# Optimization experiments

Measured on AMD Instinct MI355X. Metric: run time of the kernel, lower is better.

## Reference

```python
import jax, jax.numpy as jnp
import numpy as np

B, NQ, NKV = 16, 4096, 77
QUERY_DIM, CONTEXT_DIM = 320, 768
HEADS, DIM_HEAD = 8, 64
INNER = HEADS * DIM_HEAD
SCALE = DIM_HEAD ** (-0.5)
MAX_NEG = -jnp.finfo(jnp.float32).max / 2


def setup_inputs() -> dict:
    key = jax.random.key(0)
    ks = jax.random.split(key, 8)
    x = jax.random.normal(ks[0], (B, NQ, QUERY_DIM), dtype=jnp.float32)
    context = jax.random.normal(ks[1], (B, NKV, CONTEXT_DIM), dtype=jnp.float32)
    mask = jax.random.randint(ks[2], (B, 1, 1, NKV), 0, 2).astype(bool)
    s = 0.02
    Wq = jax.random.normal(ks[3], (QUERY_DIM, INNER), dtype=jnp.float32) * s
    Wk = jax.random.normal(ks[4], (CONTEXT_DIM, INNER), dtype=jnp.float32) * s
    Wv = jax.random.normal(ks[5], (CONTEXT_DIM, INNER), dtype=jnp.float32) * s
    Wo = jax.random.normal(ks[6], (INNER, QUERY_DIM), dtype=jnp.float32) * s
    bo = jnp.zeros((QUERY_DIM,), dtype=jnp.float32)
    return {"x": x, "context": context, "mask": mask,
            "Wq": Wq, "Wk": Wk, "Wv": Wv, "Wo": Wo, "bo": bo}


def reference(x, context, mask, Wq, Wk, Wv, Wo, bo):
    # projections (bias-free Linears)
    q = (x @ Wq).reshape(B, NQ, HEADS, DIM_HEAD)        # b q h d
    k = (context @ Wk).reshape(B, NKV, HEADS, DIM_HEAD)  # b k h d
    v = (context @ Wv).reshape(B, NKV, HEADS, DIM_HEAD)  # b k h d
    # additive mask bias: 0 where mask, -finfo.max/2 where ~mask (matches masked_fill_)
    bias = jnp.where(mask, jnp.float32(0), MAX_NEG)      # broadcast to b h q k
    sim = jnp.einsum('bqhd,bkhd->bhqk', q, k) * SCALE + bias
    attn = jax.nn.softmax(sim, axis=-1)
    out = jnp.einsum('bhqk,bkhd->bqhd', attn, v).reshape(B, NQ, INNER)
    return out @ Wo + bo  # dropout p=0 -> identity
```

## Files before the change

### kernel.cpp

```cpp
#include <hip/hip_runtime.h>

typedef unsigned short ushort_t;
typedef __attribute__((ext_vector_type(8))) short bf16x8;
typedef __attribute__((ext_vector_type(4))) float f32x4;

#define B_SZ   16
#define NQ     4096
#define NKV    77
#define QDIM   320
#define CDIM   768
#define HEADS  8
#define DHEAD  64
#define INNER  512
#define M_ROWS (B_SZ * NQ)
#define VT_STR 104

__device__ __forceinline__ ushort_t f2bf(float f) {
  unsigned u = __builtin_bit_cast(unsigned, f);
  u = (u + 0x7fffu + ((u >> 16) & 1u)) >> 16;
  return (ushort_t)u;
}

__device__ __forceinline__ void async16(const ushort_t* g, ushort_t* l) {
  __builtin_amdgcn_global_load_lds(
      (const __attribute__((address_space(1))) unsigned int*)g,
      (__attribute__((address_space(3))) unsigned int*)l,
      16, 0, 0);
}

__global__ void mask_bias_kernel(const unsigned char* __restrict__ mraw,
                                 float* __restrict__ biasT) {
  __shared__ int s_u8, s_w4;
  if (threadIdx.x == 0) { s_u8 = 0; s_w4 = 0; }
  __syncthreads();
  const int nbytes = B_SZ * NKV;
  for (int i = threadIdx.x; i < nbytes; i += blockDim.x) {
    unsigned char v = mraw[i];
    if (v && (i & 3)) atomicOr(&s_u8, 1);
    if (v && ((i & 7) == 4)) atomicOr(&s_w4, 1);
  }
  __syncthreads();
  int mode = s_u8 ? 0 : (s_w4 ? 1 : 2);
  for (int i = threadIdx.x; i < B_SZ * 80; i += blockDim.x) {
    int b = i / 80, kv = i - b * 80;
    float bias = -2e30f;
    if (kv < NKV) {
      int idx = b * NKV + kv;
      long long m;
      if (mode == 0)      m = (long long)mraw[idx];
      else if (mode == 1) m = (long long)((const int*)mraw)[idx];
      else                m = ((const long long*)mraw)[idx];
      bias = m ? 0.0f : -1e30f;
    }
    biasT[i] = bias;
  }
}

__global__ void cast_f32_bf16(const float* __restrict__ in,
                              ushort_t* __restrict__ out, int n4) {
  int i = blockIdx.x * blockDim.x + threadIdx.x;
  int stride = gridDim.x * blockDim.x;
  const float4* in4 = (const float4*)in;
  ushort4* out4 = (ushort4*)out;
  for (; i < n4; i += stride) {
    float4 v = in4[i];
    ushort4 o;
    o.x = f2bf(v.x); o.y = f2bf(v.y); o.z = f2bf(v.z); o.w = f2bf(v.w);
    out4[i] = o;
  }
}

__global__ void tcast_f32_bf16(const float* __restrict__ in,
                               ushort_t* __restrict__ out,
                               int K, int N, int Npad, float scale) {
  int i = blockIdx.x * blockDim.x + threadIdx.x;
  int stride = gridDim.x * blockDim.x;
  int total = Npad * K;
  for (; i < total; i += stride) {
    int n = i / K, k = i - n * K;
    out[i] = (n < N) ? f2bf(in[(size_t)k * N + n] * scale) : (ushort_t)0;
  }
}

__global__ void vtrans_kernel(const ushort_t* __restrict__ kvb,
                              ushort_t* __restrict__ vt) {
  const int h = blockIdx.y, b = blockIdx.z;
  const int wid = threadIdx.x >> 6, lane = threadIdx.x & 63;
  const int d = blockIdx.x * 4 + wid;
  ushort_t* dst = vt + (size_t)(b * HEADS + h) * (64 * VT_STR) + d * VT_STR;
  for (int kv = lane; kv < VT_STR; kv += 64)
    dst[kv] = (kv < NKV)
        ? kvb[(size_t)(b * NKV + kv) * 1024 + 512 + h * 64 + d]
        : (ushort_t)0;
}

__global__ __launch_bounds__(256) void gemm_bf16(
    const ushort_t* __restrict__ A, const ushort_t* __restrict__ Bt,
    ushort_t* __restrict__ Cb,
    int K, int Astride, int Bstride, int Cstride) {
  __shared__ ushort_t As[128 * 64];
  __shared__ ushort_t Bs[128 * 64];
  const int tid = threadIdx.x;
  const int wid = tid >> 6, lane = tid & 63;
  const int wr = wid >> 1, wc = wid & 1;
  const int tileM = blockIdx.x * 128, tileN = blockIdx.y * 128;

  f32x4 acc[4][4];
#pragma unroll
  for (int m = 0; m < 4; ++m)
#pragma unroll
    for (int n = 0; n < 4; ++n) acc[m][n] = (f32x4){0.f, 0.f, 0.f, 0.f};

  const int srow = lane >> 3;
  const int scol = (lane & 7) * 8;

  for (int kt = 0; kt < K; kt += 64) {
    __syncthreads();
#pragma unroll
    for (int j = 0; j < 4; ++j) {
      int s = wid * 4 + j;
      const ushort_t* ga = A + (size_t)(tileM + s * 8 + srow) * Astride + kt + scol;
      const ushort_t* gb = Bt + (size_t)(tileN + s * 8 + srow) * Bstride + kt + scol;
      async16(ga, As + s * 512);
      async16(gb, Bs + s * 512);
    }
    __syncthreads();
#pragma unroll
    for (int kc = 0; kc < 2; ++kc) {
      bf16x8 af[4], bfr[4];
#pragma unroll
      for (int m = 0; m < 4; ++m)
        af[m] = *(const bf16x8*)&As[(wr * 64 + m * 16 + (lane & 15)) * 64 + kc * 32 + (lane >> 4) * 8];
#pragma unroll
      for (int n = 0; n < 4; ++n)
        bfr[n] = *(const bf16x8*)&Bs[(wc * 64 + n * 16 + (lane & 15)) * 64 + kc * 32 + (lane >> 4) * 8];
#pragma unroll
      for (int m = 0; m < 4; ++m)
#pragma unroll
        for (int n = 0; n < 4; ++n)
          acc[m][n] = __builtin_amdgcn_mfma_f32_16x16x32_bf16(af[m], bfr[n], acc[m][n], 0, 0, 0);
    }
  }

  const int r0 = tileM + wr * 64;
  const int c0 = tileN + wc * 64;
  const int rl2 = (lane >> 4) * 4;
  const int cl = lane & 15;
#pragma unroll
  for (int m = 0; m < 4; ++m)
#pragma unroll
    for (int n = 0; n < 4; ++n) {
      int col = c0 + n * 16 + cl;
#pragma unroll
      for (int r = 0; r < 4; ++r)
        Cb[(size_t)(r0 + m * 16 + rl2 + r) * Cstride + col] = f2bf(acc[m][n][r]);
    }
}

__global__ __launch_bounds__(512, 2) void gemm_qproj(
    const float* __restrict__ x, const ushort_t* __restrict__ Wt,
    ushort_t* __restrict__ qb) {
  __shared__ ushort_t As[2][128 * 32];
  __shared__ ushort_t Bs[2][512 * 32];
  const int tid = threadIdx.x;
  const int wid = tid >> 6, lane = tid & 63;
  const int wr = wid & 1, wc = wid >> 1;
  const int rl = lane & 15, kh = (lane >> 4) * 8;
  const int tileM = blockIdx.x * 128;

  f32x4 acc[4][8];
#pragma unroll
  for (int m = 0; m < 4; ++m)
#pragma unroll
    for (int n = 0; n < 8; ++n) acc[m][n] = (f32x4){0.f, 0.f, 0.f, 0.f};

  const int arow = tid >> 3;
  const int ac4 = tid & 7;
  const float4* x4 = (const float4*)x;
  float4 pa0, pa1;

#define QP_ISSUE_A(KT)                                                        \
  {                                                                           \
    size_t base = (size_t)(tileM + arow) * 80 + ((KT) >> 2) + ac4;            \
    pa0 = x4[base];                                                           \
    pa1 = x4[base + (size_t)64 * 80];                                         \
  }
#define QP_WRITE_A(BUF)                                                       \
  {                                                                           \
    ushort4 u0, u1;                                                           \
    u0.x = f2bf(pa0.x); u0.y = f2bf(pa0.y); u0.z = f2bf(pa0.z); u0.w = f2bf(pa0.w); \
    u1.x = f2bf(pa1.x); u1.y = f2bf(pa1.y); u1.z = f2bf(pa1.z); u1.w = f2bf(pa1.w); \
    *(ushort4*)&As[BUF][arow * 32 + ac4 * 4] = u0;                            \
    *(ushort4*)&As[BUF][(arow + 64) * 32 + ac4 * 4] = u1;                     \
  }
#define QP_STAGE_B(BUF, KT)                                                   \
  _Pragma("unroll")                                                           \
  for (int i = 0; i < 4; ++i) {                                               \
    int chunk = tid + i * 512;                                                \
    int n = chunk >> 2, c8 = chunk & 3;                                       \
    async16(Wt + (size_t)n * QDIM + (KT) + c8 * 8, &Bs[BUF][chunk * 8]);      \
  }

  QP_ISSUE_A(0)
  QP_WRITE_A(0)
  QP_STAGE_B(0, 0)
  __syncthreads();

  for (int s = 0; s < 10; ++s) {
    const int cur = s & 1;
    if (s < 9) {
      QP_ISSUE_A((s + 1) * 32)
      QP_STAGE_B(cur ^ 1, (s + 1) * 32)
    }
    bf16x8 af[4], bfr[8];
#pragma unroll
    for (int m = 0; m < 4; ++m)
      af[m] = *(const bf16x8*)&As[cur][(wr * 64 + m * 16 + rl) * 32 + kh];
#pragma unroll
    for (int n = 0; n < 8; ++n)
      bfr[n] = *(const bf16x8*)&Bs[cur][(wc * 128 + n * 16 + rl) * 32 + kh];
#pragma unroll
    for (int m = 0; m < 4; ++m)
#pragma unroll
      for (int n = 0; n < 8; ++n)
        acc[m][n] = __builtin_amdgcn_mfma_f32_16x16x32_bf16(af[m], bfr[n], acc[m][n], 0, 0, 0);
    if (s < 9) QP_WRITE_A(cur ^ 1)
    __syncthreads();
  }

  const int r0 = tileM + wr * 64;
  const int c0 = wc * 128;
  const int rl2 = (lane >> 4) * 4, cl = lane & 15;
#pragma unroll
  for (int m = 0; m < 4; ++m)
#pragma unroll
    for (int n = 0; n < 8; ++n)
#pragma unroll
      for (int r = 0; r < 4; ++r)
        qb[(size_t)(r0 + m * 16 + rl2 + r) * INNER + c0 + n * 16 + cl] = f2bf(acc[m][n][r]);
}

__global__ __launch_bounds__(512, 2) void gemm_oproj(
    const ushort_t* __restrict__ A, const ushort_t* __restrict__ Wt,
    const float* __restrict__ bo, float* __restrict__ out) {
  __shared__ ushort_t As[2][128 * 64];
  __shared__ ushort_t Bs[2][384 * 64];
  const int tid = threadIdx.x;
  const int wid = tid >> 6, lane = tid & 63;
  const int wr = wid & 1, wc = wid >> 1;
  const int rl = lane & 15, kh = (lane >> 4) * 8;
  const int tileM = blockIdx.x * 128;

  f32x4 acc[4][6];
#pragma unroll
  for (int m = 0; m < 4; ++m)
#pragma unroll
    for (int n = 0; n < 6; ++n) acc[m][n] = (f32x4){0.f, 0.f, 0.f, 0.f};

#define OP_STAGE(BUF, KT)                                                     \
  _Pragma("unroll")                                                           \
  for (int i = 0; i < 2; ++i) {                                               \
    int chunk = tid + i * 512;                                                \
    int row = chunk >> 3, c8 = chunk & 7;                                     \
    async16(A + (size_t)(tileM + row) * INNER + (KT) + c8 * 8,                \
            &As[BUF][chunk * 8]);                                             \
  }                                                                           \
  _Pragma("unroll")                                                           \
  for (int i = 0; i < 6; ++i) {                                               \
    int chunk = tid + i * 512;                                                \
    int n = chunk >> 3, c8 = chunk & 7;                                       \
    async16(Wt + (size_t)n * INNER + (KT) + c8 * 8, &Bs[BUF][chunk * 8]);     \
  }

  OP_STAGE(0, 0)
  __syncthreads();

  for (int s = 0; s < 8; ++s) {
    const int cur = s & 1;
    if (s < 7) { OP_STAGE(cur ^ 1, (s + 1) * 64) }
#pragma unroll
    for (int kc = 0; kc < 2; ++kc) {
      bf16x8 af[4], bfr[6];
#pragma unroll
      for (int m = 0; m < 4; ++m)
        af[m] = *(const bf16x8*)&As[cur][(wr * 64 + m * 16 + rl) * 64 + kc * 32 + kh];
#pragma unroll
      for (int n = 0; n < 6; ++n)
        bfr[n] = *(const bf16x8*)&Bs[cur][(wc * 96 + n * 16 + rl) * 64 + kc * 32 + kh];
#pragma unroll
      for (int m = 0; m < 4; ++m)
#pragma unroll
        for (int n = 0; n < 6; ++n)
          acc[m][n] = __builtin_amdgcn_mfma_f32_16x16x32_bf16(af[m], bfr[n], acc[m][n], 0, 0, 0);
    }
    __syncthreads();
  }

  const int r0 = tileM + wr * 64;
  const int c0 = wc * 96;
  const int rl2 = (lane >> 4) * 4, cl = lane & 15;
#pragma unroll
  for (int n = 0; n < 6; ++n) {
    int col = c0 + n * 16 + cl;
    if (col < QDIM) {
      float bv = bo[col];
#pragma unroll
      for (int m = 0; m < 4; ++m)
#pragma unroll
        for (int r = 0; r < 4; ++r)
          out[(size_t)(r0 + m * 16 + rl2 + r) * QDIM + col] = acc[m][n][r] + bv;
    }
  }
}

__global__ __launch_bounds__(256) void attn_kernel(
    const ushort_t* __restrict__ qb, const ushort_t* __restrict__ kvb,
    const ushort_t* __restrict__ vt, const float* __restrict__ biasT,
    ushort_t* __restrict__ ab) {
  __shared__ ushort_t Vt[64 * VT_STR];
  __shared__ ushort_t P[4 * 16 * VT_STR];
  const int qt = blockIdx.x, h = blockIdx.y, b = blockIdx.z;
  const int tid = threadIdx.x, wid = tid >> 6, lane = tid & 63;
  const int rl = lane & 15;
  const int kh = (lane >> 4) * 8;

  const ushort_t* vtg = vt + (size_t)(b * HEADS + h) * (64 * VT_STR);
  for (int i = tid; i < 832; i += 256) async16(vtg + i * 8, Vt + i * 8);
  for (int i = tid; i < 832; i += 256)
    *(bf16x8*)&P[i * 8] = (bf16x8){0, 0, 0, 0, 0, 0, 0, 0};

  bf16x8 kf[5][2];
  float bias_v[5];
#pragma unroll
  for (int nt = 0; nt < 5; ++nt) {
    int kv = nt * 16 + rl;
    bias_v[nt] = biasT[b * 80 + kv];
    kf[nt][0] = (bf16x8){0, 0, 0, 0, 0, 0, 0, 0};
    kf[nt][1] = (bf16x8){0, 0, 0, 0, 0, 0, 0, 0};
    if (kv < NKV) {
      const ushort_t* kp = &kvb[(size_t)(b * NKV + kv) * 1024 + h * 64 + kh];
      kf[nt][0] = *(const bf16x8*)kp;
      kf[nt][1] = *(const bf16x8*)(kp + 32);
    }
  }
  __syncthreads();

  const int qbase = b * NQ + qt * 256;
  const int pbase = wid * (16 * VT_STR);
#pragma unroll 1
  for (int chunk = 0; chunk < 4; ++chunk) {
    if (chunk) __syncthreads();
    const int row0 = chunk * 64 + wid * 16;

    const ushort_t* qp = &qb[(size_t)(qbase + row0 + rl) * INNER + h * 64 + kh];
    bf16x8 qf0 = *(const bf16x8*)qp;
    bf16x8 qf1 = *(const bf16x8*)(qp + 32);

    f32x4 s[5];
#pragma unroll
    for (int nt = 0; nt < 5; ++nt) {
      s[nt] = (f32x4){0.f, 0.f, 0.f, 0.f};
      s[nt] = __builtin_amdgcn_mfma_f32_16x16x32_bf16(qf0, kf[nt][0], s[nt], 0, 0, 0);
      s[nt] = __builtin_amdgcn_mfma_f32_16x16x32_bf16(qf1, kf[nt][1], s[nt], 0, 0, 0);
    }

    float mx[4] = {-3.0e38f, -3.0e38f, -3.0e38f, -3.0e38f};
#pragma unroll
    for (int nt = 0; nt < 5; ++nt)
#pragma unroll
      for (int r = 0; r < 4; ++r) {
        float v = s[nt][r] + bias_v[nt];
        s[nt][r] = v;
        mx[r] = fmaxf(mx[r], v);
      }
#pragma unroll
    for (int d = 1; d < 16; d <<= 1)
#pragma unroll
      for (int r = 0; r < 4; ++r) mx[r] = fmaxf(mx[r], __shfl_xor(mx[r], d, 64));

    float sm[4] = {0.f, 0.f, 0.f, 0.f};
#pragma unroll
    for (int nt = 0; nt < 5; ++nt)
#pragma unroll
      for (int r = 0; r < 4; ++r) {
        float p = __expf(s[nt][r] - mx[r]);
        s[nt][r] = p;
        sm[r] += p;
      }
#pragma unroll
    for (int d = 1; d < 16; d <<= 1)
#pragma unroll
      for (int r = 0; r < 4; ++r) sm[r] += __shfl_xor(sm[r], d, 64);

    float rcp[4];
#pragma unroll
    for (int r = 0; r < 4; ++r) rcp[r] = 1.0f / sm[r];

#pragma unroll
    for (int nt = 0; nt < 5; ++nt)
#pragma unroll
      for (int r = 0; r < 4; ++r)
        P[pbase + ((lane >> 4) * 4 + r) * VT_STR + nt * 16 + rl] = f2bf(s[nt][r]);

    f32x4 o[4];
#pragma unroll
    for (int n = 0; n < 4; ++n) o[n] = (f32x4){0.f, 0.f, 0.f, 0.f};
#pragma unroll
    for (int kc = 0; kc < 3; ++kc) {
      bf16x8 pf = *(const bf16x8*)&P[pbase + rl * VT_STR + kc * 32 + kh];
#pragma unroll
      for (int n = 0; n < 4; ++n) {
        bf16x8 vf = *(const bf16x8*)&Vt[(n * 16 + rl) * VT_STR + kc * 32 + kh];
        o[n] = __builtin_amdgcn_mfma_f32_16x16x32_bf16(pf, vf, o[n], 0, 0, 0);
      }
    }

#pragma unroll
    for (int n = 0; n < 4; ++n)
#pragma unroll
      for (int r = 0; r < 4; ++r)
        P[pbase + ((lane >> 4) * 4 + r) * VT_STR + n * 16 + rl] = f2bf(o[n][r] * rcp[r]);

    __syncthreads();

    {
      const int rflat = tid >> 2, d0 = (tid & 3) * 16;
      const ushort_t* src = &P[(rflat >> 4) * (16 * VT_STR) + (rflat & 15) * VT_STR + d0];
      ushort_t* dst = &ab[(size_t)(qbase + chunk * 64 + rflat) * INNER + h * 64 + d0];
      *(bf16x8*)dst = *(const bf16x8*)src;
      *(bf16x8*)(dst + 8) = *(const bf16x8*)(src + 8);
    }
  }
}

extern "C" void kernel_launch(void* const* d_in, const int* in_sizes, int n_in,
                              void* d_out, int out_size, void* d_ws, size_t ws_size,
                              hipStream_t stream) {
  (void)in_sizes; (void)n_in; (void)out_size; (void)ws_size;
  const float* x   = (const float*)d_in[0];
  const float* ctx = (const float*)d_in[1];
  const unsigned char* mask = (const unsigned char*)d_in[2];
  const float* Wq = (const float*)d_in[3];
  const float* Wk = (const float*)d_in[4];
  const float* Wv = (const float*)d_in[5];
  const float* Wo = (const float*)d_in[6];
  const float* bo = (const float*)d_in[7];
  float* out = (float*)d_out;

  char* ws = (char*)d_ws;
  size_t off = 0;
  auto alloc = [&](size_t bytes) {
    char* p = ws + off;
    off += (bytes + 255) & ~(size_t)255;
    return p;
  };
  float*    biasT = (float*)alloc(B_SZ * 80 * sizeof(float));
  ushort_t* ab    = (ushort_t*)alloc((size_t)M_ROWS * INNER * 2);
  ushort_t* qb    = (ushort_t*)alloc((size_t)M_ROWS * INNER * 2);
  ushort_t* cb    = (ushort_t*)alloc((size_t)1280 * CDIM * 2);
  ushort_t* Wqb   = (ushort_t*)alloc((size_t)INNER * QDIM * 2);
  ushort_t* Wkvb  = (ushort_t*)alloc((size_t)1024 * CDIM * 2);
  ushort_t* Wob   = (ushort_t*)alloc((size_t)384 * INNER * 2);
  ushort_t* kvb   = (ushort_t*)alloc((size_t)1280 * 1024 * 2);
  ushort_t* vt    = (ushort_t*)alloc((size_t)B_SZ * HEADS * 64 * VT_STR * 2);

  mask_bias_kernel<<<1, 256, 0, stream>>>(mask, biasT);
  cast_f32_bf16<<<512, 256, 0, stream>>>(ctx, cb, B_SZ * NKV * CDIM / 4);
  tcast_f32_bf16<<<640, 256, 0, stream>>>(Wq, Wqb, QDIM, INNER, INNER, 0.125f);
  tcast_f32_bf16<<<1536, 256, 0, stream>>>(Wk, Wkvb, CDIM, INNER, INNER, 1.0f);
  tcast_f32_bf16<<<1536, 256, 0, stream>>>(Wv, Wkvb + (size_t)INNER * CDIM, CDIM, INNER, INNER, 1.0f);
  tcast_f32_bf16<<<768, 256, 0, stream>>>(Wo, Wob, INNER, QDIM, 384, 1.0f);

  gemm_qproj<<<M_ROWS / 128, 512, 0, stream>>>(x, Wqb, qb);
  dim3 g2(1280 / 128, 1024 / 128);
  gemm_bf16<<<g2, 256, 0, stream>>>(cb, Wkvb, kvb, CDIM, CDIM, CDIM, 1024);
  vtrans_kernel<<<dim3(16, HEADS, B_SZ), 256, 0, stream>>>(kvb, vt);
  attn_kernel<<<dim3(NQ / 256, HEADS, B_SZ), 256, 0, stream>>>(qb, kvb, vt, biasT, ab);
  gemm_oproj<<<M_ROWS / 128, 512, 0, stream>>>(ab, Wob, bo, out);
}
```

Before: 191.9 us.

## Restructure Q projection to keep weights in registers and stream fp32 x via LDS

Replaces the Q-projection GEMM with a weight-stationary kernel. Each wave holds a 32-column slice of Wq for the full K=320 in registers, while fp32 rows of x are copied asynchronously into a swizzled LDS tile and converted to bf16 with packed cvt instructions at fragment load. The grid now splits N into 4 blocks of 128 columns, so each block reads only a quarter of the weights but x tiles are re-read 4 times across blocks. Loads are no longer double-buffered, so each 32-row chunk waits on its load before computing, and the per-block MFMA work per barrier is small.

```diff
diff --git a/kernel.cpp b/kernel.cpp
--- a/kernel.cpp
+++ b/kernel.cpp
@@ -157,87 +157,90 @@
     }
 }
 
-__global__ __launch_bounds__(512, 2) void gemm_qproj(
+__global__ __launch_bounds__(256, 2) void gemm_qproj_ws(
     const float* __restrict__ x, const ushort_t* __restrict__ Wt,
     ushort_t* __restrict__ qb) {
-  __shared__ ushort_t As[2][128 * 32];
-  __shared__ ushort_t Bs[2][512 * 32];
-  const int tid = threadIdx.x;
-  const int wid = tid >> 6, lane = tid & 63;
-  const int wr = wid & 1, wc = wid >> 1;
-  const int rl = lane & 15, kh = (lane >> 4) * 8;
-  const int tileM = blockIdx.x * 128;
-
-  f32x4 acc[4][8];
-#pragma unroll
-  for (int m = 0; m < 4; ++m)
-#pragma unroll
-    for (int n = 0; n < 8; ++n) acc[m][n] = (f32x4){0.f, 0.f, 0.f, 0.f};
-
-  const int arow = tid >> 3;
-  const int ac4 = tid & 7;
-  const float4* x4 = (const float4*)x;
-  float4 pa0, pa1;
-
-#define QP_ISSUE_A(KT)                                                        \
-  {                                                                           \
-    size_t base = (size_t)(tileM + arow) * 80 + ((KT) >> 2) + ac4;            \
-    pa0 = x4[base];                                                           \
-    pa1 = x4[base + (size_t)64 * 80];                                         \
-  }
-#define QP_WRITE_A(BUF)                                                       \
-  {                                                                           \
-    ushort4 u0, u1;                                                           \
-    u0.x = f2bf(pa0.x); u0.y = f2bf(pa0.y); u0.z = f2bf(pa0.z); u0.w = f2bf(pa0.w); \
-    u1.x = f2bf(pa1.x); u1.y = f2bf(pa1.y); u1.z = f2bf(pa1.z); u1.w = f2bf(pa1.w); \
-    *(ushort4*)&As[BUF][arow * 32 + ac4 * 4] = u0;                            \
-    *(ushort4*)&As[BUF][(arow + 64) * 32 + ac4 * 4] = u1;                     \
-  }
-#define QP_STAGE_B(BUF, KT)                                                   \
-  _Pragma("unroll")                                                           \
-  for (int i = 0; i < 4; ++i) {                                               \
-    int chunk = tid + i * 512;                                                \
-    int n = chunk >> 2, c8 = chunk & 3;                                       \
-    async16(Wt + (size_t)n * QDIM + (KT) + c8 * 8, &Bs[BUF][chunk * 8]);      \
-  }
-
-  QP_ISSUE_A(0)
-  QP_WRITE_A(0)
-  QP_STAGE_B(0, 0)
-  __syncthreads();
-
-  for (int s = 0; s < 10; ++s) {
-    const int cur = s & 1;
-    if (s < 9) {
-      QP_ISSUE_A((s + 1) * 32)
-      QP_STAGE_B(cur ^ 1, (s + 1) * 32)
-    }
-    bf16x8 af[4], bfr[8];
-#pragma unroll
-    for (int m = 0; m < 4; ++m)
-      af[m] = *(const bf16x8*)&As[cur][(wr * 64 + m * 16 + rl) * 32 + kh];
-#pragma unroll
-    for (int n = 0; n < 8; ++n)
-      bfr[n] = *(const bf16x8*)&Bs[cur][(wc * 128 + n * 16 + rl) * 32 + kh];
-#pragma unroll
-    for (int m = 0; m < 4; ++m)
-#pragma unroll
-      for (int n = 0; n < 8; ++n)
-        acc[m][n] = __builtin_amdgcn_mfma_f32_16x16x32_bf16(af[m], bfr[n], acc[m][n], 0, 0, 0);
-    if (s < 9) QP_WRITE_A(cur ^ 1)
+  __shared__ __align__(16) float As[32 * 320];
+  const int tid = threadIdx.x, wid = tid >> 6, lane = tid & 63;
+  const int rl = lane & 15, g = lane >> 4;
+  const int nbase = blockIdx.y * 128 + wid * 32;
+  const size_t Mbase = (size_t)blockIdx.x * 128;
+
+  bf16x8 bf[2][10];
+#pragma unroll
+  for (int n = 0; n < 2; ++n)
+#pragma unroll
+    for (int kc = 0; kc < 10; ++kc)
+      bf[n][kc] = *(const bf16x8*)&Wt[(size_t)(nbase + n * 16 + rl) * QDIM + kc * 32 + g * 8];
+
+  unsigned off[10];
+#pragma unroll
+  for (int i = 0; i < 10; ++i) {
+    unsigned p = wid * 10240 + i * 1024 + lane * 16;
+    unsigned row = p / 1280u;
+    unsigned rem = p - row * 1280u;
+    off[i] = (unsigned)((Mbase + row) * 1280u) + (rem ^ ((row & 7u) << 4));
+  }
+
+  const char* xB = (const char*)x;
+  char* AsB = (char*)As;
+
+  for (int it = 0; it < 4; ++it) {
+#pragma unroll
+    for (int i = 0; i < 10; ++i)
+      async16((const ushort_t*)(xB + off[i]),
+              (ushort_t*)(AsB + wid * 10240 + i * 1024));
     __syncthreads();
-  }
-
-  const int r0 = tileM + wr * 64;
-  const int c0 = wc * 128;
-  const int rl2 = (lane >> 4) * 4, cl = lane & 15;
-#pragma unroll
-  for (int m = 0; m < 4; ++m)
-#pragma unroll
-    for (int n = 0; n < 8; ++n)
-#pragma unroll
-      for (int r = 0; r < 4; ++r)
-        qb[(size_t)(r0 + m * 16 + rl2 + r) * INNER + c0 + n * 16 + cl] = f2bf(acc[m][n][r]);
+
+    f32x4 acc[2][2];
+#pragma unroll
+    for (int m = 0; m < 2; ++m)
+#pragma unroll
+      for (int n = 0; n < 2; ++n) acc[m][n] = (f32x4){0.f, 0.f, 0.f, 0.f};
+
+#pragma unroll
+    for (int kc = 0; kc < 10; ++kc) {
+      bf16x8 af[2];
+#pragma unroll
+      for (int m = 0; m < 2; ++m) {
+        const int row = m * 16 + rl;
+        const int cb = kc * 128 + g * 32;
+        const int s = (row & 7) << 4;
+        f32x4 lo = *(const f32x4*)(AsB + row * 1280 + (cb ^ s));
+        f32x4 hi = *(const f32x4*)(AsB + row * 1280 + ((cb + 16) ^ s));
+        unsigned w0, w1, w2, w3;
+        asm("v_cvt_pk_bf16_f32 %0, %1, %2" : "=v"(w0) : "v"(lo[0]), "v"(lo[1]));
+        asm("v_cvt_pk_bf16_f32 %0, %1, %2" : "=v"(w1) : "v"(lo[2]), "v"(lo[3]));
+        asm("v_cvt_pk_bf16_f32 %0, %1, %2" : "=v"(w2) : "v"(hi[0]), "v"(hi[1]));
+        asm("v_cvt_pk_bf16_f32 %0, %1, %2" : "=v"(w3) : "v"(hi[2]), "v"(hi[3]));
+        union { unsigned u[4]; bf16x8 v; } cv;
+        cv.u[0] = w0; cv.u[1] = w1; cv.u[2] = w2; cv.u[3] = w3;
+        af[m] = cv.v;
+      }
+#pragma unroll
+      for (int m = 0; m < 2; ++m)
+#pragma unroll
+        for (int n = 0; n < 2; ++n)
+          acc[m][n] = __builtin_amdgcn_mfma_f32_16x16x32_bf16(af[m], bf[n][kc], acc[m][n], 0, 0, 0);
+    }
+
+    const size_t r0 = Mbase + it * 32;
+#pragma unroll
+    for (int m = 0; m < 2; ++m)
+#pragma unroll
+      for (int n = 0; n < 2; ++n) {
+        const int col = nbase + n * 16 + rl;
+#pragma unroll
+        for (int r = 0; r < 4; ++r)
+          qb[(r0 + m * 16 + g * 4 + r) * INNER + col] = f2bf(acc[m][n][r]);
+      }
+
+    if (it < 3) {
+      __syncthreads();
+#pragma unroll
+      for (int i = 0; i < 10; ++i) off[i] += 32 * 1280;
+    }
+  }
 }
 
 __global__ __launch_bounds__(512, 2) void gemm_oproj(
@@ -471,7 +474,7 @@
   tcast_f32_bf16<<<1536, 256, 0, stream>>>(Wv, Wkvb + (size_t)INNER * CDIM, CDIM, INNER, INNER, 1.0f);
   tcast_f32_bf16<<<768, 256, 0, stream>>>(Wo, Wob, INNER, QDIM, 384, 1.0f);
 
-  gemm_qproj<<<M_ROWS / 128, 512, 0, stream>>>(x, Wqb, qb);
+  gemm_qproj_ws<<<dim3(M_ROWS / 128, 4), 256, 0, stream>>>(x, Wqb, qb);
   dim3 g2(1280 / 128, 1024 / 128);
   gemm_bf16<<<g2, 256, 0, stream>>>(cb, Wkvb, kvb, CDIM, CDIM, CDIM, 1024);
   vtrans_kernel<<<dim3(16, HEADS, B_SZ), 256, 0, stream>>>(kvb, vt);
```

Result: slower. 210.6 us (+9.7%).
